# Kernel tuning notes

Measured on AMD Instinct MI355X. Metric: run time of the kernel, lower is better.

Reference implementation:

```python
import jax, jax.numpy as jnp
import numpy as np

B, S, D_MODEL = 2, 2048, 1024
N_HEADS, N_KV_HEADS, D_HEAD = 16, 4, 64
N_GROUPS = N_HEADS // N_KV_HEADS
ATTN_SCALE = 1.0 / np.sqrt(D_HEAD)  # qk_scale_factor=1.0
LOGIT_SOFTCAP = 15.0
WINDOW = 256
N_GLOBAL = 4
EPS = 1e-8


def _l2_normalize(x):
    norm = jnp.linalg.norm(x, axis=-1, keepdims=True)
    return x / (norm + EPS)


def _apply_rope(t, cos, sin):
    # t: (B, H, S, D); cos/sin: (S, D//2)
    half = t.shape[-1] // 2
    x1, x2 = t[..., :half], t[..., half:]
    c = cos[None, None, :, :]
    s = sin[None, None, :, :]
    return jnp.concatenate([x1 * c - x2 * s, x1 * s + x2 * c], axis=-1)


def _sliding_window_mask(seq_len, window, n_global):
    q = jnp.arange(seq_len)[:, None]
    k = jnp.arange(seq_len)[None, :]
    causal = k <= q
    in_window = k > q - window
    is_global = k < n_global
    return (causal & in_window | is_global)[None, None, :, :]


def setup_inputs() -> dict:
    key = jax.random.key(0)
    ks = jax.random.split(key, 7)
    x = jax.random.normal(ks[0], (B, S, D_MODEL), dtype=jnp.float32)
    # RoPE tables from standard inverse-frequency construction
    inv_freq = 1.0 / (10000.0 ** (jnp.arange(0, D_HEAD, 2, dtype=jnp.float32) / D_HEAD))
    angles = jnp.arange(S, dtype=jnp.float32)[:, None] * inv_freq[None, :]  # (S, D_HEAD//2)
    cos = jnp.cos(angles)
    sin = jnp.sin(angles)
    # causal mask supplied by caller (TransformerLM): (1,1,S,S) bool, True = attend
    mask = (jnp.arange(S)[None, :] <= jnp.arange(S)[:, None])[None, None, :, :]
    scale_in = 1.0 / np.sqrt(D_MODEL)
    Wq = jax.random.normal(ks[1], (D_MODEL, N_HEADS * D_HEAD), dtype=jnp.float32) * scale_in
    Wk = jax.random.normal(ks[2], (D_MODEL, N_KV_HEADS * D_HEAD), dtype=jnp.float32) * scale_in
    Wv = jax.random.normal(ks[3], (D_MODEL, N_KV_HEADS * D_HEAD), dtype=jnp.float32) * scale_in
    Wo = jax.random.normal(ks[4], (N_HEADS * D_HEAD, D_MODEL), dtype=jnp.float32) * (1.0 / np.sqrt(N_HEADS * D_HEAD))
    return {"x": x, "cos": cos, "sin": sin, "mask": mask, "Wq": Wq, "Wk": Wk, "Wv": Wv, "Wo": Wo}


def reference(x, cos, sin, mask, Wq, Wk, Wv, Wo):
    Bb, Ss, _ = x.shape
    q = (x @ Wq).reshape(Bb, Ss, N_HEADS, D_HEAD).transpose(0, 2, 1, 3)      # (B,H,S,D)
    k = (x @ Wk).reshape(Bb, Ss, N_KV_HEADS, D_HEAD).transpose(0, 2, 1, 3)   # (B,Hkv,S,D)
    v = (x @ Wv).reshape(Bb, Ss, N_KV_HEADS, D_HEAD).transpose(0, 2, 1, 3)
    # QK L2 normalization (in fp32)
    q = _l2_normalize(q.astype(jnp.float32)).astype(q.dtype)
    k = _l2_normalize(k.astype(jnp.float32)).astype(k.dtype)
    # RoPE
    q = _apply_rope(q, cos, sin)
    k = _apply_rope(k, cos, sin)
    # GQA: expand kv heads
    k_exp = jnp.repeat(k, N_GROUPS, axis=1)
    v_exp = jnp.repeat(v, N_GROUPS, axis=1)
    scores = jnp.einsum('bhqd,bhkd->bhqk', q.astype(jnp.float32), k_exp.astype(jnp.float32)) * ATTN_SCALE
    scores = LOGIT_SOFTCAP * jnp.tanh(scores / LOGIT_SOFTCAP)
    window_mask = _sliding_window_mask(Ss, WINDOW, N_GLOBAL)
    combined = mask & window_mask
    scores = jnp.where(combined, scores, jnp.float32(-1e9))
    weights = jax.nn.softmax(scores, axis=-1)
    context = jnp.einsum('bhqk,bhkd->bhqd', weights, v_exp.astype(jnp.float32))
    context = context.transpose(0, 2, 1, 3).reshape(Bb, Ss, N_HEADS * D_HEAD).astype(x.dtype)
    return context @ Wo
```

## Files before the change

### kernel.cpp

```cpp
#include <hip/hip_runtime.h>
#include <hip/hip_bf16.h>

#define BATCH 2
#define SLEN 2048
#define DMODEL 1024
#define NHEADS 16
#define NKV 4
#define DHEAD 64
#define WINDOW 256
#define NGLOBAL 4

typedef __attribute__((ext_vector_type(8))) short short8;
typedef __attribute__((ext_vector_type(4))) float floatx4;

__device__ __forceinline__ ushort f2bf(float f) {
    __hip_bfloat16 h = __float2bfloat16(f);
    return *reinterpret_cast<ushort*>(&h);
}
__device__ __forceinline__ float bf2f(ushort u) {
    __hip_bfloat16 h = *reinterpret_cast<__hip_bfloat16*>(&u);
    return __bfloat162float(h);
}
__device__ __forceinline__ bool is_bf16_inputs(const uint* cosu) {
    return (cosu[0] & 0xFFFFu) != 0u;
}
__device__ __forceinline__ void gload_lds16(const ushort* g, ushort* l) {
    __builtin_amdgcn_global_load_lds(
        (const __attribute__((address_space(1))) void*)g,
        (__attribute__((address_space(3))) void*)l, 16, 0, 0);
}

__device__ __forceinline__ void stage_row(const ushort* gbase, size_t gstride, int k0,
                                          ushort* lds, int call, int lane) {
    const int c2 = call * 64 + lane;
    const int srow = c2 / 9;
    const int rem = c2 - srow * 9;
    const int colu = (rem == 8) ? 0 : rem * 8;
    gload_lds16(&gbase[(size_t)srow * gstride + k0 + colu], &lds[call * 512]);
}

__global__ __launch_bounds__(256) void prep_all(const void* __restrict__ x,
                                                const void* __restrict__ cosi,
                                                const void* __restrict__ sini,
                                                const void* __restrict__ Wq,
                                                const void* __restrict__ Wk,
                                                const void* __restrict__ Wv,
                                                const void* __restrict__ Wo,
                                                ushort* __restrict__ xb,
                                                float* __restrict__ cosf,
                                                float* __restrict__ sinf,
                                                ushort* __restrict__ Wt,
                                                ushort* __restrict__ Wot,
                                                const uint* __restrict__ cosu)
{
    __shared__ ushort t[32][33];
    const bool isbf = is_bf16_inputs(cosu);
    const int bid = blockIdx.x, tid = threadIdx.x;
    if (bid < 2048) {
        size_t i = (size_t)bid * 256 + tid;
        size_t e = i * 8;
        if (isbf) {
            *reinterpret_cast<uint4*>(xb + e) = reinterpret_cast<const uint4*>(x)[i];
        } else {
            const float* f = reinterpret_cast<const float*>(x) + e;
            ushort o[8];
#pragma unroll
            for (int j = 0; j < 8; ++j) o[j] = f2bf(f[j]);
            *reinterpret_cast<uint4*>(xb + e) = *reinterpret_cast<uint4*>(o);
        }
        return;
    }
    if (bid < 2560) {
        int i = (bid - 2048) * 256 + tid;
        const void* src = (i < SLEN * 32) ? cosi : sini;
        float* dst = (i < SLEN * 32) ? cosf : sinf;
        int e = i & (SLEN * 32 - 1);
        dst[e] = isbf ? bf2f(reinterpret_cast<const ushort*>(src)[e])
                      : reinterpret_cast<const float*>(src)[e];
        return;
    }
    const void* src; ushort* dst; int C, tl;
    if (bid < 3584)      { src = Wq; dst = Wt;                       C = 1024; tl = bid - 2560; }
    else if (bid < 3840) { src = Wk; dst = Wt + (size_t)1024 * 1024; C = 256;  tl = bid - 3584; }
    else if (bid < 4096) { src = Wv; dst = Wt + (size_t)1280 * 1024; C = 256;  tl = bid - 3840; }
    else                 { src = Wo; dst = Wot;                      C = 1024; tl = bid - 4096; }
    const int nbx = C >> 5;
    const int bx = (tl % nbx) * 32, by = (tl / nbx) * 32;
    const int tx = tid & 31, ty = tid >> 5;
#pragma unroll
    for (int j = 0; j < 32; j += 8) {
        size_t idx = (size_t)(by + ty + j) * C + bx + tx;
        t[ty + j][tx] = isbf ? reinterpret_cast<const ushort*>(src)[idx]
                             : f2bf(reinterpret_cast<const float*>(src)[idx]);
    }
    __syncthreads();
#pragma unroll
    for (int j = 0; j < 32; j += 8)
        dst[(size_t)(bx + ty + j) * 1024 + by + tx] = t[tx][ty + j];
}

__global__ __launch_bounds__(256) void gemm_qkv_nr(const ushort* __restrict__ A,
                                                   const ushort* __restrict__ Bt,
                                                   const float* __restrict__ cosf,
                                                   const float* __restrict__ sinf,
                                                   ushort* __restrict__ Qb,
                                                   ushort* __restrict__ Kg,
                                                   ushort* __restrict__ Vtg)
{
    __shared__ __align__(16) ushort sm[13824];
    ushort* lsA = sm;
    ushort* lsB = sm + 9216;
    const int tid = threadIdx.x;
    const int lane = tid & 63, w = tid >> 6;
    const int ln15 = lane & 15, quad = lane >> 4;
    const int z = blockIdx.x;
    const int rm = blockIdx.y * 128;
    const int cn = z * 64;

    floatx4 acc[2][4];
#pragma unroll
    for (int i = 0; i < 2; ++i)
#pragma unroll
        for (int j = 0; j < 4; ++j) acc[i][j] = (floatx4){0.f, 0.f, 0.f, 0.f};

    const ushort* Ab = A + (size_t)rm * 1024;
    const ushort* Bb = Bt + (size_t)cn * 1024;

    for (int k0 = 0; k0 < 1024; k0 += 64) {
        __syncthreads();
#pragma unroll
        for (int i = 0; i < 5; ++i) {
            const int call = i * 4 + w;
            if (call < 18) stage_row(Ab, 1024, k0, lsA, call, lane);
        }
#pragma unroll
        for (int i = 0; i < 3; ++i) {
            const int call = i * 4 + w;
            if (call < 9) stage_row(Bb, 1024, k0, lsB, call, lane);
        }
        __syncthreads();
#pragma unroll
        for (int kk = 0; kk < 64; kk += 32) {
            short8 af[2], bv[4];
#pragma unroll
            for (int i = 0; i < 2; ++i)
                af[i] = *reinterpret_cast<const short8*>(&lsA[(w * 32 + i * 16 + ln15) * 72 + kk + quad * 8]);
#pragma unroll
            for (int j = 0; j < 4; ++j)
                bv[j] = *reinterpret_cast<const short8*>(&lsB[(j * 16 + ln15) * 72 + kk + quad * 8]);
#pragma unroll
            for (int i = 0; i < 2; ++i)
#pragma unroll
                for (int j = 0; j < 4; ++j)
                    acc[i][j] = __builtin_amdgcn_mfma_f32_16x16x32_bf16(af[i], bv[j], acc[i][j], 0, 0, 0);
        }
    }

    __syncthreads();
    const int b = rm >> 11, s0 = rm & (SLEN - 1);
    if (z < 20) {
#pragma unroll
        for (int i = 0; i < 2; ++i) {
#pragma unroll
            for (int r = 0; r < 4; ++r) {
                const int row_l = w * 32 + i * 16 + quad * 4 + r;
                float v0 = acc[i][0][r], v1 = acc[i][1][r], v2 = acc[i][2][r], v3 = acc[i][3][r];
                float ss = v0 * v0 + v1 * v1 + v2 * v2 + v3 * v3;
                ss += __shfl_xor(ss, 1, 64);
                ss += __shfl_xor(ss, 2, 64);
                ss += __shfl_xor(ss, 4, 64);
                ss += __shfl_xor(ss, 8, 64);
                const float inv = 1.f / (sqrtf(ss) + 1e-8f);
                const float n0 = v0 * inv, n1 = v1 * inv, n2 = v2 * inv, n3 = v3 * inv;
                const int spos = s0 + row_l;
                const float c0 = cosf[spos * 32 + ln15],  c1 = cosf[spos * 32 + 16 + ln15];
                const float sn0 = sinf[spos * 32 + ln15], sn1 = sinf[spos * 32 + 16 + ln15];
                sm[row_l * 72 + ln15]      = f2bf(n0 * c0 - n2 * sn0);
                sm[row_l * 72 + 16 + ln15] = f2bf(n1 * c1 - n3 * sn1);
                sm[row_l * 72 + 32 + ln15] = f2bf(n0 * sn0 + n2 * c0);
                sm[row_l * 72 + 48 + ln15] = f2bf(n1 * sn1 + n3 * c1);
            }
        }
        __syncthreads();
        ushort* dst = (z < 16) ? Qb + ((size_t)(b * NHEADS + z) * SLEN + s0) * 64
                               : Kg + ((size_t)(b * NKV + (z - 16)) * SLEN + s0) * 64;
#pragma unroll
        for (int it = 0; it < 4; ++it) {
            const int c = it * 256 + tid;
            const int row = c >> 3, col = (c & 7) * 8;
            *reinterpret_cast<uint4*>(dst + (size_t)row * 64 + col) =
                *reinterpret_cast<const uint4*>(&sm[row * 72 + col]);
        }
    } else {
#pragma unroll
        for (int i = 0; i < 2; ++i)
#pragma unroll
            for (int r = 0; r < 4; ++r) {
                const int row_l = w * 32 + i * 16 + quad * 4 + r;
#pragma unroll
                for (int j = 0; j < 4; ++j)
                    sm[(j * 16 + ln15) * 136 + row_l] = f2bf(acc[i][j][r]);
            }
        __syncthreads();
        ushort* dst = Vtg + ((size_t)(b * NKV + (z - 20)) * 64) * SLEN;
#pragma unroll
        for (int it = 0; it < 4; ++it) {
            const int c = it * 256 + tid;
            const int d = c >> 4, sb = (c & 15) * 8;
            *reinterpret_cast<uint4*>(dst + (size_t)d * SLEN + s0 + sb) =
                *reinterpret_cast<const uint4*>(&sm[d * 136 + sb]);
        }
    }
}

__global__ __launch_bounds__(256) void attn_mfma(const ushort* __restrict__ Qb,
                                                 const ushort* __restrict__ Kg,
                                                 const ushort* __restrict__ Vtg,
                                                 ushort* __restrict__ ctx)
{
    __shared__ ushort Ks[64 * 72];
    __shared__ ushort Vs[64 * 72];
    __shared__ ushort Ps[4][16 * 72];

    const int tid = threadIdx.x;
    const int lane = tid & 63, w = tid >> 6;
    const int ln15 = lane & 15, quad = lane >> 4;
    const int bid = blockIdx.x;
    const int qt = bid & 31, bh = bid >> 5;
    const int h = bh & (NHEADS - 1), b = bh >> 4, hkv = h >> 2;
    const int q0 = qt * 64;
    const int qw = q0 + w * 16;

    const ushort* Qrow = Qb + ((size_t)bh * SLEN + qw) * 64;
    const ushort* Kbase = Kg + (size_t)(b * NKV + hkv) * SLEN * 64;
    const ushort* Vbase = Vtg + (size_t)(b * NKV + hkv) * 64 * SLEN;

    short8 qf0 = *reinterpret_cast<const short8*>(Qrow + (size_t)ln15 * 64 + quad * 8);
    short8 qf1 = *reinterpret_cast<const short8*>(Qrow + (size_t)ln15 * 64 + 32 + quad * 8);

    floatx4 O0 = {0,0,0,0}, O1 = {0,0,0,0}, O2 = {0,0,0,0}, O3 = {0,0,0,0};
    float lp[4] = {0.f, 0.f, 0.f, 0.f};

    int kminA = q0 - (WINDOW - 1); if (kminA < 0) kminA = 0;
    kminA &= ~63;
    const int gmax = kminA < NGLOBAL ? kminA : NGLOBAL;
    const int nc = (q0 + 64 - kminA) >> 6;

    for (int c = (gmax > 0 ? -1 : 0); c < nc; ++c) {
        const int kbase = (c < 0) ? 0 : kminA + c * 64;
        __syncthreads();
#pragma unroll
        for (int j = 0; j < 2; ++j) {
            const int c2 = tid + j * 256;
            const int row = c2 >> 3, col = (c2 & 7) * 8;
            *reinterpret_cast<uint4*>(&Ks[row * 72 + col]) =
                *reinterpret_cast<const uint4*>(&Kbase[(size_t)(kbase + row) * 64 + col]);
            *reinterpret_cast<uint4*>(&Vs[row * 72 + col]) =
                *reinterpret_cast<const uint4*>(&Vbase[(size_t)row * SLEN + kbase + col]);
        }
        __syncthreads();

#pragma unroll
        for (int t = 0; t < 4; ++t) {
            short8 kf0 = *reinterpret_cast<const short8*>(&Ks[(t * 16 + ln15) * 72 + quad * 8]);
            short8 kf1 = *reinterpret_cast<const short8*>(&Ks[(t * 16 + ln15) * 72 + 32 + quad * 8]);
            floatx4 sc = {0,0,0,0};
            sc = __builtin_amdgcn_mfma_f32_16x16x32_bf16(qf0, kf0, sc, 0, 0, 0);
            sc = __builtin_amdgcn_mfma_f32_16x16x32_bf16(qf1, kf1, sc, 0, 0, 0);
            const int k = kbase + t * 16 + ln15;
#pragma unroll
            for (int r = 0; r < 4; ++r) {
                const int q = qw + quad * 4 + r;
                const bool valid = (c < 0) ? (k < gmax)
                                           : (k <= q && (k + WINDOW > q || k < NGLOBAL));
                float sv = sc[r] * 0.125f;
                float st = sv - sv * sv * sv * (1.0f / 675.0f);
                float p = __expf(st);
                Ps[w][(quad * 4 + r) * 72 + t * 16 + ln15] = valid ? f2bf(p) : (ushort)0;
                lp[r] += valid ? p : 0.f;
            }
        }
        short8 af0 = *reinterpret_cast<const short8*>(&Ps[w][ln15 * 72 + quad * 8]);
        short8 af1 = *reinterpret_cast<const short8*>(&Ps[w][ln15 * 72 + 32 + quad * 8]);
#pragma unroll
        for (int n = 0; n < 4; ++n) {
            short8 vf0 = *reinterpret_cast<const short8*>(&Vs[(n * 16 + ln15) * 72 + quad * 8]);
            short8 vf1 = *reinterpret_cast<const short8*>(&Vs[(n * 16 + ln15) * 72 + 32 + quad * 8]);
            floatx4 On = (n == 0) ? O0 : (n == 1) ? O1 : (n == 2) ? O2 : O3;
            On = __builtin_amdgcn_mfma_f32_16x16x32_bf16(af0, vf0, On, 0, 0, 0);
            On = __builtin_amdgcn_mfma_f32_16x16x32_bf16(af1, vf1, On, 0, 0, 0);
            if (n == 0) O0 = On; else if (n == 1) O1 = On; else if (n == 2) O2 = On; else O3 = On;
        }
    }

#pragma unroll
    for (int r = 0; r < 4; ++r) {
#pragma unroll
        for (int off = 1; off < 16; off <<= 1)
            lp[r] += __shfl_xor(lp[r], off, 64);
        const float inv = __builtin_amdgcn_rcpf(lp[r]);
        const int q = qw + quad * 4 + r;
        ushort* crow = ctx + ((size_t)(b * SLEN + q)) * DMODEL + h * 64 + ln15;
        crow[0]  = f2bf(O0[r] * inv);
        crow[16] = f2bf(O1[r] * inv);
        crow[32] = f2bf(O2[r] * inv);
        crow[48] = f2bf(O3[r] * inv);
    }
}

__global__ __launch_bounds__(256) void gemm_out(const ushort* __restrict__ A,
                                                const ushort* __restrict__ Bt,
                                                void* __restrict__ out,
                                                const uint* __restrict__ cosu)
{
    __shared__ __align__(16) ushort sm[13824];
    ushort* lsA = sm;
    ushort* lsB = sm + 9216;
    const int tid = threadIdx.x;
    const int lane = tid & 63, w = tid >> 6;
    const int ln15 = lane & 15, quad = lane >> 4;
    const int rm = blockIdx.y * 128;
    const int cn = blockIdx.x * 64;

    floatx4 acc[2][4];
#pragma unroll
    for (int i = 0; i < 2; ++i)
#pragma unroll
        for (int j = 0; j < 4; ++j) acc[i][j] = (floatx4){0.f, 0.f, 0.f, 0.f};

    const ushort* Ab = A + (size_t)rm * 1024;
    const ushort* Bb = Bt + (size_t)cn * 1024;

    for (int k0 = 0; k0 < 1024; k0 += 64) {
        __syncthreads();
#pragma unroll
        for (int i = 0; i < 5; ++i) {
            const int call = i * 4 + w;
            if (call < 18) stage_row(Ab, 1024, k0, lsA, call, lane);
        }
#pragma unroll
        for (int i = 0; i < 3; ++i) {
            const int call = i * 4 + w;
            if (call < 9) stage_row(Bb, 1024, k0, lsB, call, lane);
        }
        __syncthreads();
#pragma unroll
        for (int kk = 0; kk < 64; kk += 32) {
            short8 af[2], bv[4];
#pragma unroll
            for (int i = 0; i < 2; ++i)
                af[i] = *reinterpret_cast<const short8*>(&lsA[(w * 32 + i * 16 + ln15) * 72 + kk + quad * 8]);
#pragma unroll
            for (int j = 0; j < 4; ++j)
                bv[j] = *reinterpret_cast<const short8*>(&lsB[(j * 16 + ln15) * 72 + kk + quad * 8]);
#pragma unroll
            for (int i = 0; i < 2; ++i)
#pragma unroll
                for (int j = 0; j < 4; ++j)
                    acc[i][j] = __builtin_amdgcn_mfma_f32_16x16x32_bf16(af[i], bv[j], acc[i][j], 0, 0, 0);
        }
    }

    const bool outbf = is_bf16_inputs(cosu);
#pragma unroll
    for (int i = 0; i < 2; ++i) {
#pragma unroll
        for (int r = 0; r < 4; ++r) {
            const int grow = rm + w * 32 + i * 16 + quad * 4 + r;
#pragma unroll
            for (int j = 0; j < 4; ++j) {
                const int gcol = cn + j * 16 + ln15;
                if (outbf) reinterpret_cast<ushort*>(out)[(size_t)grow * DMODEL + gcol] = f2bf(acc[i][j][r]);
                else       reinterpret_cast<float*>(out)[(size_t)grow * DMODEL + gcol] = acc[i][j][r];
            }
        }
    }
}

extern "C" void kernel_launch(void* const* d_in, const int* in_sizes, int n_in,
                              void* d_out, int out_size, void* d_ws, size_t ws_size,
                              hipStream_t stream)
{
    (void)in_sizes; (void)n_in; (void)out_size; (void)ws_size;
    const void* x = d_in[0];
    const void* cosi = d_in[1];
    const void* sini = d_in[2];
    const uint* cosu = (const uint*)d_in[1];
    const void* Wq = d_in[4];
    const void* Wk = d_in[5];
    const void* Wv = d_in[6];
    const void* Wo = d_in[7];

    ushort* xb = (ushort*)d_ws;
    ushort* Wt = xb + (size_t)4096 * 1024;
    ushort* Wot = Wt + (size_t)1536 * 1024;
    float* cosf = (float*)(Wot + (size_t)1024 * 1024);
    float* sinf = cosf + (size_t)SLEN * 32;
    ushort* Qbf = (ushort*)(sinf + (size_t)SLEN * 32);
    ushort* Kgf = Qbf + (size_t)BATCH * NHEADS * SLEN * 64;
    ushort* Vtg = Kgf + (size_t)BATCH * NKV * SLEN * 64;
    ushort* ctx = Vtg + (size_t)BATCH * NKV * 64 * SLEN;

    prep_all<<<dim3(5120), 256, 0, stream>>>(x, cosi, sini, Wq, Wk, Wv, Wo,
                                             xb, cosf, sinf, Wt, Wot, cosu);

    gemm_qkv_nr<<<dim3(24, 32), 256, 0, stream>>>(xb, Wt, cosf, sinf, Qbf, Kgf, Vtg);

    attn_mfma<<<dim3(BATCH * NHEADS * SLEN / 64), 256, 0, stream>>>(Qbf, Kgf, Vtg, ctx);

    gemm_out<<<dim3(16, 32), 256, 0, stream>>>(ctx, Wot, d_out, cosu);
}
```

Measured before the change: 155.1 us.

## Fuse input conversion and weight transpose into GEMMs, add unmasked fast path in attention

Removes the separate prep kernel that converted x, cos/sin and the weights to bf16 and transposed the weights. The QKV and output GEMMs now read the fp32 inputs directly, converting and transposing tiles into LDS as they load them, and the RoPE epilogue reads cos/sin directly. The attention kernel stages K/V with async global-to-LDS loads and takes a mask-free path for fully valid tiles. This saves a kernel launch and a round trip through workspace memory, but the fp32 loads are uncoalesced and scalar. The transposed LDS stores may hit bank conflicts, and every GEMM block now repeats the conversion work.

```diff
diff --git a/kernel.cpp b/kernel.cpp
--- a/kernel.cpp
+++ b/kernel.cpp
@@ -39,73 +39,33 @@
     gload_lds16(&gbase[(size_t)srow * gstride + k0 + colu], &lds[call * 512]);
 }
 
-__global__ __launch_bounds__(256) void prep_all(const void* __restrict__ x,
-                                                const void* __restrict__ cosi,
-                                                const void* __restrict__ sini,
-                                                const void* __restrict__ Wq,
-                                                const void* __restrict__ Wk,
-                                                const void* __restrict__ Wv,
-                                                const void* __restrict__ Wo,
-                                                ushort* __restrict__ xb,
-                                                float* __restrict__ cosf,
-                                                float* __restrict__ sinf,
-                                                ushort* __restrict__ Wt,
-                                                ushort* __restrict__ Wot,
-                                                const uint* __restrict__ cosu)
-{
-    __shared__ ushort t[32][33];
-    const bool isbf = is_bf16_inputs(cosu);
-    const int bid = blockIdx.x, tid = threadIdx.x;
-    if (bid < 2048) {
-        size_t i = (size_t)bid * 256 + tid;
-        size_t e = i * 8;
-        if (isbf) {
-            *reinterpret_cast<uint4*>(xb + e) = reinterpret_cast<const uint4*>(x)[i];
-        } else {
-            const float* f = reinterpret_cast<const float*>(x) + e;
-            ushort o[8];
-#pragma unroll
-            for (int j = 0; j < 8; ++j) o[j] = f2bf(f[j]);
-            *reinterpret_cast<uint4*>(xb + e) = *reinterpret_cast<uint4*>(o);
-        }
-        return;
-    }
-    if (bid < 2560) {
-        int i = (bid - 2048) * 256 + tid;
-        const void* src = (i < SLEN * 32) ? cosi : sini;
-        float* dst = (i < SLEN * 32) ? cosf : sinf;
-        int e = i & (SLEN * 32 - 1);
-        dst[e] = isbf ? bf2f(reinterpret_cast<const ushort*>(src)[e])
-                      : reinterpret_cast<const float*>(src)[e];
-        return;
-    }
-    const void* src; ushort* dst; int C, tl;
-    if (bid < 3584)      { src = Wq; dst = Wt;                       C = 1024; tl = bid - 2560; }
-    else if (bid < 3840) { src = Wk; dst = Wt + (size_t)1024 * 1024; C = 256;  tl = bid - 3584; }
-    else if (bid < 4096) { src = Wv; dst = Wt + (size_t)1280 * 1024; C = 256;  tl = bid - 3840; }
-    else                 { src = Wo; dst = Wot;                      C = 1024; tl = bid - 4096; }
-    const int nbx = C >> 5;
-    const int bx = (tl % nbx) * 32, by = (tl / nbx) * 32;
-    const int tx = tid & 31, ty = tid >> 5;
-#pragma unroll
-    for (int j = 0; j < 32; j += 8) {
-        size_t idx = (size_t)(by + ty + j) * C + bx + tx;
-        t[ty + j][tx] = isbf ? reinterpret_cast<const ushort*>(src)[idx]
-                             : f2bf(reinterpret_cast<const float*>(src)[idx]);
-    }
-    __syncthreads();
-#pragma unroll
-    for (int j = 0; j < 32; j += 8)
-        dst[(size_t)(bx + ty + j) * 1024 + by + tx] = t[tx][ty + j];
-}
-
-__global__ __launch_bounds__(256) void gemm_qkv_nr(const ushort* __restrict__ A,
-                                                   const ushort* __restrict__ Bt,
-                                                   const float* __restrict__ cosf,
-                                                   const float* __restrict__ sinf,
+__device__ __forceinline__ void stage_wT(const void* W, bool isbf, int N, int cn,
+                                         int k0, int ncol, int lane, ushort* lsB) {
+    ushort v[8];
+    if (isbf) {
+        const ushort* Ws = reinterpret_cast<const ushort*>(W);
+        uint4 raw = *reinterpret_cast<const uint4*>(&Ws[(size_t)(k0 + lane) * N + cn + ncol]);
+        *reinterpret_cast<uint4*>(v) = raw;
+    } else {
+        const float* Wf = reinterpret_cast<const float*>(W);
+        const float* p = &Wf[(size_t)(k0 + lane) * N + cn + ncol];
+#pragma unroll
+        for (int i = 0; i < 8; ++i) v[i] = f2bf(p[i]);
+    }
+#pragma unroll
+    for (int i = 0; i < 8; ++i) lsB[(ncol + i) * 72 + lane] = v[i];
+}
+
+__global__ __launch_bounds__(256) void gemm_qkv_nr(const void* __restrict__ x,
+                                                   const void* __restrict__ cosi,
+                                                   const void* __restrict__ sini,
+                                                   const void* __restrict__ Wq,
+                                                   const void* __restrict__ Wk,
+                                                   const void* __restrict__ Wv,
                                                    ushort* __restrict__ Qb,
                                                    ushort* __restrict__ Kg,
-                                                   ushort* __restrict__ Vtg)
+                                                   ushort* __restrict__ Vtg,
+                                                   const uint* __restrict__ cosu)
 {
     __shared__ __align__(16) ushort sm[13824];
     ushort* lsA = sm;
@@ -115,7 +75,12 @@
     const int ln15 = lane & 15, quad = lane >> 4;
     const int z = blockIdx.x;
     const int rm = blockIdx.y * 128;
-    const int cn = z * 64;
+    const bool isbf = is_bf16_inputs(cosu);
+
+    const void* Wsrc; int N, cn;
+    if (z < 16)      { Wsrc = Wq; N = 1024; cn = z * 64; }
+    else if (z < 20) { Wsrc = Wk; N = 256;  cn = (z - 16) * 64; }
+    else             { Wsrc = Wv; N = 256;  cn = (z - 20) * 64; }
 
     floatx4 acc[2][4];
 #pragma unroll
@@ -123,21 +88,31 @@
 #pragma unroll
         for (int j = 0; j < 4; ++j) acc[i][j] = (floatx4){0.f, 0.f, 0.f, 0.f};
 
-    const ushort* Ab = A + (size_t)rm * 1024;
-    const ushort* Bb = Bt + (size_t)cn * 1024;
+    const ushort* xb16 = reinterpret_cast<const ushort*>(x) + (size_t)rm * 1024;
+    const float* xf32 = reinterpret_cast<const float*>(x) + (size_t)rm * 1024;
 
     for (int k0 = 0; k0 < 1024; k0 += 64) {
         __syncthreads();
-#pragma unroll
-        for (int i = 0; i < 5; ++i) {
-            const int call = i * 4 + w;
-            if (call < 18) stage_row(Ab, 1024, k0, lsA, call, lane);
-        }
-#pragma unroll
-        for (int i = 0; i < 3; ++i) {
-            const int call = i * 4 + w;
-            if (call < 9) stage_row(Bb, 1024, k0, lsB, call, lane);
-        }
+        if (isbf) {
+#pragma unroll
+            for (int i = 0; i < 5; ++i) {
+                const int call = i * 4 + w;
+                if (call < 18) stage_row(xb16, 1024, k0, lsA, call, lane);
+            }
+        } else {
+#pragma unroll
+            for (int j = 0; j < 4; ++j) {
+                const int c = tid + j * 256;
+                const int srow = c >> 3, col = (c & 7) * 8;
+                const float* p = &xf32[(size_t)srow * 1024 + k0 + col];
+                ushort o[8];
+#pragma unroll
+                for (int i = 0; i < 8; ++i) o[i] = f2bf(p[i]);
+                *reinterpret_cast<uint4*>(&lsA[srow * 72 + col]) = *reinterpret_cast<uint4*>(o);
+            }
+        }
+        stage_wT(Wsrc, isbf, N, cn, k0, w * 8, lane, lsB);
+        stage_wT(Wsrc, isbf, N, cn, k0, (w + 4) * 8, lane, lsB);
         __syncthreads();
 #pragma unroll
         for (int kk = 0; kk < 64; kk += 32) {
@@ -159,6 +134,10 @@
     __syncthreads();
     const int b = rm >> 11, s0 = rm & (SLEN - 1);
     if (z < 20) {
+        const ushort* cosb = reinterpret_cast<const ushort*>(cosi);
+        const ushort* sinb = reinterpret_cast<const ushort*>(sini);
+        const float* cosF = reinterpret_cast<const float*>(cosi);
+        const float* sinF = reinterpret_cast<const float*>(sini);
 #pragma unroll
         for (int i = 0; i < 2; ++i) {
 #pragma unroll
@@ -173,8 +152,14 @@
                 const float inv = 1.f / (sqrtf(ss) + 1e-8f);
                 const float n0 = v0 * inv, n1 = v1 * inv, n2 = v2 * inv, n3 = v3 * inv;
                 const int spos = s0 + row_l;
-                const float c0 = cosf[spos * 32 + ln15],  c1 = cosf[spos * 32 + 16 + ln15];
-                const float sn0 = sinf[spos * 32 + ln15], sn1 = sinf[spos * 32 + 16 + ln15];
+                float c0, c1, sn0, sn1;
+                if (isbf) {
+                    c0 = bf2f(cosb[spos * 32 + ln15]);  c1 = bf2f(cosb[spos * 32 + 16 + ln15]);
+                    sn0 = bf2f(sinb[spos * 32 + ln15]); sn1 = bf2f(sinb[spos * 32 + 16 + ln15]);
+                } else {
+                    c0 = cosF[spos * 32 + ln15];  c1 = cosF[spos * 32 + 16 + ln15];
+                    sn0 = sinF[spos * 32 + ln15]; sn1 = sinF[spos * 32 + 16 + ln15];
+                }
                 sm[row_l * 72 + ln15]      = f2bf(n0 * c0 - n2 * sn0);
                 sm[row_l * 72 + 16 + ln15] = f2bf(n1 * c1 - n3 * sn1);
                 sm[row_l * 72 + 32 + ln15] = f2bf(n0 * sn0 + n2 * c0);
@@ -218,13 +203,13 @@
                                                  const ushort* __restrict__ Vtg,
                                                  ushort* __restrict__ ctx)
 {
-    __shared__ ushort Ks[64 * 72];
-    __shared__ ushort Vs[64 * 72];
-    __shared__ ushort Ps[4][16 * 72];
-
+    __shared__ __align__(16) ushort sm[13824];
+    ushort* Ks = sm;
+    ushort* Vs = sm + 4608;
     const int tid = threadIdx.x;
     const int lane = tid & 63, w = tid >> 6;
     const int ln15 = lane & 15, quad = lane >> 4;
+    ushort* Ps = sm + 9216 + w * 1152;
     const int bid = blockIdx.x;
     const int qt = bid & 31, bh = bid >> 5;
     const int h = bh & (NHEADS - 1), b = bh >> 4, hkv = h >> 2;
@@ -250,38 +235,59 @@
         const int kbase = (c < 0) ? 0 : kminA + c * 64;
         __syncthreads();
 #pragma unroll
-        for (int j = 0; j < 2; ++j) {
-            const int c2 = tid + j * 256;
-            const int row = c2 >> 3, col = (c2 & 7) * 8;
-            *reinterpret_cast<uint4*>(&Ks[row * 72 + col]) =
-                *reinterpret_cast<const uint4*>(&Kbase[(size_t)(kbase + row) * 64 + col]);
-            *reinterpret_cast<uint4*>(&Vs[row * 72 + col]) =
-                *reinterpret_cast<const uint4*>(&Vbase[(size_t)row * SLEN + kbase + col]);
-        }
-        __syncthreads();
-
-#pragma unroll
-        for (int t = 0; t < 4; ++t) {
-            short8 kf0 = *reinterpret_cast<const short8*>(&Ks[(t * 16 + ln15) * 72 + quad * 8]);
-            short8 kf1 = *reinterpret_cast<const short8*>(&Ks[(t * 16 + ln15) * 72 + 32 + quad * 8]);
-            floatx4 sc = {0,0,0,0};
-            sc = __builtin_amdgcn_mfma_f32_16x16x32_bf16(qf0, kf0, sc, 0, 0, 0);
-            sc = __builtin_amdgcn_mfma_f32_16x16x32_bf16(qf1, kf1, sc, 0, 0, 0);
-            const int k = kbase + t * 16 + ln15;
-#pragma unroll
-            for (int r = 0; r < 4; ++r) {
-                const int q = qw + quad * 4 + r;
-                const bool valid = (c < 0) ? (k < gmax)
-                                           : (k <= q && (k + WINDOW > q || k < NGLOBAL));
-                float sv = sc[r] * 0.125f;
-                float st = sv - sv * sv * sv * (1.0f / 675.0f);
-                float p = __expf(st);
-                Ps[w][(quad * 4 + r) * 72 + t * 16 + ln15] = valid ? f2bf(p) : (ushort)0;
-                lp[r] += valid ? p : 0.f;
-            }
-        }
-        short8 af0 = *reinterpret_cast<const short8*>(&Ps[w][ln15 * 72 + quad * 8]);
-        short8 af1 = *reinterpret_cast<const short8*>(&Ps[w][ln15 * 72 + 32 + quad * 8]);
+        for (int i = 0; i < 3; ++i) {
+            const int call = i * 4 + w;
+            if (call < 9) stage_row(Kbase + (size_t)kbase * 64, 64, 0, Ks, call, lane);
+        }
+#pragma unroll
+        for (int i = 0; i < 3; ++i) {
+            const int call = i * 4 + w;
+            if (call < 9) stage_row(Vbase + kbase, SLEN, 0, Vs, call, lane);
+        }
+        __syncthreads();
+
+        const bool allvalid = (c >= 0) && (kbase + 63 <= qw) && (kbase + WINDOW >= qw + 16);
+        if (allvalid) {
+#pragma unroll
+            for (int t = 0; t < 4; ++t) {
+                short8 kf0 = *reinterpret_cast<const short8*>(&Ks[(t * 16 + ln15) * 72 + quad * 8]);
+                short8 kf1 = *reinterpret_cast<const short8*>(&Ks[(t * 16 + ln15) * 72 + 32 + quad * 8]);
+                floatx4 sc = {0,0,0,0};
+                sc = __builtin_amdgcn_mfma_f32_16x16x32_bf16(qf0, kf0, sc, 0, 0, 0);
+                sc = __builtin_amdgcn_mfma_f32_16x16x32_bf16(qf1, kf1, sc, 0, 0, 0);
+#pragma unroll
+                for (int r = 0; r < 4; ++r) {
+                    float sv = sc[r] * 0.125f;
+                    float st = sv - sv * sv * sv * (1.0f / 675.0f);
+                    float p = __expf(st);
+                    Ps[(quad * 4 + r) * 72 + t * 16 + ln15] = f2bf(p);
+                    lp[r] += p;
+                }
+            }
+        } else {
+#pragma unroll
+            for (int t = 0; t < 4; ++t) {
+                short8 kf0 = *reinterpret_cast<const short8*>(&Ks[(t * 16 + ln15) * 72 + quad * 8]);
+                short8 kf1 = *reinterpret_cast<const short8*>(&Ks[(t * 16 + ln15) * 72 + 32 + quad * 8]);
+                floatx4 sc = {0,0,0,0};
+                sc = __builtin_amdgcn_mfma_f32_16x16x32_bf16(qf0, kf0, sc, 0, 0, 0);
+                sc = __builtin_amdgcn_mfma_f32_16x16x32_bf16(qf1, kf1, sc, 0, 0, 0);
+                const int k = kbase + t * 16 + ln15;
+#pragma unroll
+                for (int r = 0; r < 4; ++r) {
+                    const int q = qw + quad * 4 + r;
+                    const bool valid = (c < 0) ? (k < gmax)
+                                               : (k <= q && (k + WINDOW > q || k < NGLOBAL));
+                    float sv = sc[r] * 0.125f;
+                    float st = sv - sv * sv * sv * (1.0f / 675.0f);
+                    float p = __expf(st);
+                    Ps[(quad * 4 + r) * 72 + t * 16 + ln15] = valid ? f2bf(p) : (ushort)0;
+                    lp[r] += valid ? p : 0.f;
+                }
+            }
+        }
+        short8 af0 = *reinterpret_cast<const short8*>(&Ps[ln15 * 72 + quad * 8]);
+        short8 af1 = *reinterpret_cast<const short8*>(&Ps[ln15 * 72 + 32 + quad * 8]);
 #pragma unroll
         for (int n = 0; n < 4; ++n) {
             short8 vf0 = *reinterpret_cast<const short8*>(&Vs[(n * 16 + ln15) * 72 + quad * 8]);
@@ -309,7 +315,7 @@
 }
 
 __global__ __launch_bounds__(256) void gemm_out(const ushort* __restrict__ A,
-                                                const ushort* __restrict__ Bt,
+                                                const void* __restrict__ Wo,
                                                 void* __restrict__ out,
                                                 const uint* __restrict__ cosu)
 {
@@ -321,6 +327,7 @@
     const int ln15 = lane & 15, quad = lane >> 4;
     const int rm = blockIdx.y * 128;
     const int cn = blockIdx.x * 64;
+    const bool isbf = is_bf16_inputs(cosu);
 
     floatx4 acc[2][4];
 #pragma unroll
@@ -329,7 +336,6 @@
         for (int j = 0; j < 4; ++j) acc[i][j] = (floatx4){0.f, 0.f, 0.f, 0.f};
 
     const ushort* Ab = A + (size_t)rm * 1024;
-    const ushort* Bb = Bt + (size_t)cn * 1024;
 
     for (int k0 = 0; k0 < 1024; k0 += 64) {
         __syncthreads();
@@ -338,11 +344,8 @@
             const int call = i * 4 + w;
             if (call < 18) stage_row(Ab, 1024, k0, lsA, call, lane);
         }
-#pragma unroll
-        for (int i = 0; i < 3; ++i) {
-            const int call = i * 4 + w;
-            if (call < 9) stage_row(Bb, 1024, k0, lsB, call, lane);
-        }
+        stage_wT(Wo, isbf, 1024, cn, k0, w * 8, lane, lsB);
+        stage_wT(Wo, isbf, 1024, cn, k0, (w + 4) * 8, lane, lsB);
         __syncthreads();
 #pragma unroll
         for (int kk = 0; kk < 64; kk += 32) {
@@ -361,7 +364,6 @@
         }
     }
 
-    const bool outbf = is_bf16_inputs(cosu);
 #pragma unroll
     for (int i = 0; i < 2; ++i) {
 #pragma unroll
@@ -370,8 +372,8 @@
 #pragma unroll
             for (int j = 0; j < 4; ++j) {
                 const int gcol = cn + j * 16 + ln15;
-                if (outbf) reinterpret_cast<ushort*>(out)[(size_t)grow * DMODEL + gcol] = f2bf(acc[i][j][r]);
-                else       reinterpret_cast<float*>(out)[(size_t)grow * DMODEL + gcol] = acc[i][j][r];
+                if (isbf) reinterpret_cast<ushort*>(out)[(size_t)grow * DMODEL + gcol] = f2bf(acc[i][j][r]);
+                else      reinterpret_cast<float*>(out)[(size_t)grow * DMODEL + gcol] = acc[i][j][r];
             }
         }
     }
@@ -391,22 +393,15 @@
     const void* Wv = d_in[6];
     const void* Wo = d_in[7];
 
-    ushort* xb = (ushort*)d_ws;
-    ushort* Wt = xb + (size_t)4096 * 1024;
-    ushort* Wot = Wt + (size_t)1536 * 1024;
-    float* cosf = (float*)(Wot + (size_t)1024 * 1024);
-    float* sinf = cosf + (size_t)SLEN * 32;
-    ushort* Qbf = (ushort*)(sinf + (size_t)SLEN * 32);
+    ushort* Qbf = (ushort*)d_ws;
     ushort* Kgf = Qbf + (size_t)BATCH * NHEADS * SLEN * 64;
     ushort* Vtg = Kgf + (size_t)BATCH * NKV * SLEN * 64;
     ushort* ctx = Vtg + (size_t)BATCH * NKV * 64 * SLEN;
 
-    prep_all<<<dim3(5120), 256, 0, stream>>>(x, cosi, sini, Wq, Wk, Wv, Wo,
-                                             xb, cosf, sinf, Wt, Wot, cosu);
-
-    gemm_qkv_nr<<<dim3(24, 32), 256, 0, stream>>>(xb, Wt, cosf, sinf, Qbf, Kgf, Vtg);
+    gemm_qkv_nr<<<dim3(24, 32), 256, 0, stream>>>(x, cosi, sini, Wq, Wk, Wv,
+                                                  Qbf, Kgf, Vtg, cosu);
 
     attn_mfma<<<dim3(BATCH * NHEADS * SLEN / 64), 256, 0, stream>>>(Qbf, Kgf, Vtg, ctx);
 
-    gemm_out<<<dim3(16, 32), 256, 0, stream>>>(ctx, Wot, d_out, cosu);
-}
+    gemm_out<<<dim3(16, 32), 256, 0, stream>>>(ctx, Wo, d_out, cosu);
+}
```

Measured after the change: 186.8 us. 1.2x slower.

## Skip x copy for bf16 inputs, use stage_row in attention, fast path unmasked tiles

Applied to the files above, without the earlier changes.

When the inputs are bf16, the prep kernel no longer copies x into a workspace buffer, and the QKV GEMM reads x directly. The attention kernel now stages K and V tiles with the shared stage_row helper and a unified shared-memory buffer. It also adds a branch that skips per-element mask evaluation for tiles that are entirely inside the causal window. The inputs are fp32 by default, so the x-copy skip likely does not run. The mask fast path adds code size and divergence risk.

```diff
diff --git a/kernel.cpp b/kernel.cpp
--- a/kernel.cpp
+++ b/kernel.cpp
@@ -57,17 +57,14 @@
     const bool isbf = is_bf16_inputs(cosu);
     const int bid = blockIdx.x, tid = threadIdx.x;
     if (bid < 2048) {
+        if (isbf) return;
         size_t i = (size_t)bid * 256 + tid;
         size_t e = i * 8;
-        if (isbf) {
-            *reinterpret_cast<uint4*>(xb + e) = reinterpret_cast<const uint4*>(x)[i];
-        } else {
-            const float* f = reinterpret_cast<const float*>(x) + e;
-            ushort o[8];
-#pragma unroll
-            for (int j = 0; j < 8; ++j) o[j] = f2bf(f[j]);
-            *reinterpret_cast<uint4*>(xb + e) = *reinterpret_cast<uint4*>(o);
-        }
+        const float* f = reinterpret_cast<const float*>(x) + e;
+        ushort o[8];
+#pragma unroll
+        for (int j = 0; j < 8; ++j) o[j] = f2bf(f[j]);
+        *reinterpret_cast<uint4*>(xb + e) = *reinterpret_cast<uint4*>(o);
         return;
     }
     if (bid < 2560) {
@@ -99,13 +96,15 @@
         dst[(size_t)(bx + ty + j) * 1024 + by + tx] = t[tx][ty + j];
 }
 
-__global__ __launch_bounds__(256) void gemm_qkv_nr(const ushort* __restrict__ A,
+__global__ __launch_bounds__(256) void gemm_qkv_nr(const void* __restrict__ x,
+                                                   const ushort* __restrict__ xb,
                                                    const ushort* __restrict__ Bt,
                                                    const float* __restrict__ cosf,
                                                    const float* __restrict__ sinf,
                                                    ushort* __restrict__ Qb,
                                                    ushort* __restrict__ Kg,
-                                                   ushort* __restrict__ Vtg)
+                                                   ushort* __restrict__ Vtg,
+                                                   const uint* __restrict__ cosu)
 {
     __shared__ __align__(16) ushort sm[13824];
     ushort* lsA = sm;
@@ -116,6 +115,7 @@
     const int z = blockIdx.x;
     const int rm = blockIdx.y * 128;
     const int cn = z * 64;
+    const bool isbf = is_bf16_inputs(cosu);
 
     floatx4 acc[2][4];
 #pragma unroll
@@ -123,7 +123,7 @@
 #pragma unroll
         for (int j = 0; j < 4; ++j) acc[i][j] = (floatx4){0.f, 0.f, 0.f, 0.f};
 
-    const ushort* Ab = A + (size_t)rm * 1024;
+    const ushort* Ab = (isbf ? reinterpret_cast<const ushort*>(x) : xb) + (size_t)rm * 1024;
     const ushort* Bb = Bt + (size_t)cn * 1024;
 
     for (int k0 = 0; k0 < 1024; k0 += 64) {
@@ -218,13 +218,13 @@
                                                  const ushort* __restrict__ Vtg,
                                                  ushort* __restrict__ ctx)
 {
-    __shared__ ushort Ks[64 * 72];
-    __shared__ ushort Vs[64 * 72];
-    __shared__ ushort Ps[4][16 * 72];
-
+    __shared__ __align__(16) ushort sm[13824];
+    ushort* Ks = sm;
+    ushort* Vs = sm + 4608;
     const int tid = threadIdx.x;
     const int lane = tid & 63, w = tid >> 6;
     const int ln15 = lane & 15, quad = lane >> 4;
+    ushort* Ps = sm + 9216 + w * 1152;
     const int bid = blockIdx.x;
     const int qt = bid & 31, bh = bid >> 5;
     const int h = bh & (NHEADS - 1), b = bh >> 4, hkv = h >> 2;
@@ -250,38 +250,59 @@
         const int kbase = (c < 0) ? 0 : kminA + c * 64;
         __syncthreads();
 #pragma unroll
-        for (int j = 0; j < 2; ++j) {
-            const int c2 = tid + j * 256;
-            const int row = c2 >> 3, col = (c2 & 7) * 8;
-            *reinterpret_cast<uint4*>(&Ks[row * 72 + col]) =
-                *reinterpret_cast<const uint4*>(&Kbase[(size_t)(kbase + row) * 64 + col]);
-            *reinterpret_cast<uint4*>(&Vs[row * 72 + col]) =
-                *reinterpret_cast<const uint4*>(&Vbase[(size_t)row * SLEN + kbase + col]);
-        }
-        __syncthreads();
-
-#pragma unroll
-        for (int t = 0; t < 4; ++t) {
-            short8 kf0 = *reinterpret_cast<const short8*>(&Ks[(t * 16 + ln15) * 72 + quad * 8]);
-            short8 kf1 = *reinterpret_cast<const short8*>(&Ks[(t * 16 + ln15) * 72 + 32 + quad * 8]);
-            floatx4 sc = {0,0,0,0};
-            sc = __builtin_amdgcn_mfma_f32_16x16x32_bf16(qf0, kf0, sc, 0, 0, 0);
-            sc = __builtin_amdgcn_mfma_f32_16x16x32_bf16(qf1, kf1, sc, 0, 0, 0);
-            const int k = kbase + t * 16 + ln15;
-#pragma unroll
-            for (int r = 0; r < 4; ++r) {
-                const int q = qw + quad * 4 + r;
-                const bool valid = (c < 0) ? (k < gmax)
-                                           : (k <= q && (k + WINDOW > q || k < NGLOBAL));
-                float sv = sc[r] * 0.125f;
-                float st = sv - sv * sv * sv * (1.0f / 675.0f);
-                float p = __expf(st);
-                Ps[w][(quad * 4 + r) * 72 + t * 16 + ln15] = valid ? f2bf(p) : (ushort)0;
-                lp[r] += valid ? p : 0.f;
+        for (int i = 0; i < 3; ++i) {
+            const int call = i * 4 + w;
+            if (call < 9) stage_row(Kbase + (size_t)kbase * 64, 64, 0, Ks, call, lane);
+        }
+#pragma unroll
+        for (int i = 0; i < 3; ++i) {
+            const int call = i * 4 + w;
+            if (call < 9) stage_row(Vbase + kbase, SLEN, 0, Vs, call, lane);
+        }
+        __syncthreads();
+
+        const bool allvalid = (c >= 0) && (kbase + 63 <= qw) && (kbase + WINDOW >= qw + 16);
+        if (allvalid) {
+#pragma unroll
+            for (int t = 0; t < 4; ++t) {
+                short8 kf0 = *reinterpret_cast<const short8*>(&Ks[(t * 16 + ln15) * 72 + quad * 8]);
+                short8 kf1 = *reinterpret_cast<const short8*>(&Ks[(t * 16 + ln15) * 72 + 32 + quad * 8]);
+                floatx4 sc = {0,0,0,0};
+                sc = __builtin_amdgcn_mfma_f32_16x16x32_bf16(qf0, kf0, sc, 0, 0, 0);
+                sc = __builtin_amdgcn_mfma_f32_16x16x32_bf16(qf1, kf1, sc, 0, 0, 0);
+#pragma unroll
+                for (int r = 0; r < 4; ++r) {
+                    float sv = sc[r] * 0.125f;
+                    float st = sv - sv * sv * sv * (1.0f / 675.0f);
+                    float p = __expf(st);
+                    Ps[(quad * 4 + r) * 72 + t * 16 + ln15] = f2bf(p);
+                    lp[r] += p;
+                }
             }
-        }
-        short8 af0 = *reinterpret_cast<const short8*>(&Ps[w][ln15 * 72 + quad * 8]);
-        short8 af1 = *reinterpret_cast<const short8*>(&Ps[w][ln15 * 72 + 32 + quad * 8]);
+        } else {
+#pragma unroll
+            for (int t = 0; t < 4; ++t) {
+                short8 kf0 = *reinterpret_cast<const short8*>(&Ks[(t * 16 + ln15) * 72 + quad * 8]);
+                short8 kf1 = *reinterpret_cast<const short8*>(&Ks[(t * 16 + ln15) * 72 + 32 + quad * 8]);
+                floatx4 sc = {0,0,0,0};
+                sc = __builtin_amdgcn_mfma_f32_16x16x32_bf16(qf0, kf0, sc, 0, 0, 0);
+                sc = __builtin_amdgcn_mfma_f32_16x16x32_bf16(qf1, kf1, sc, 0, 0, 0);
+                const int k = kbase + t * 16 + ln15;
+#pragma unroll
+                for (int r = 0; r < 4; ++r) {
+                    const int q = qw + quad * 4 + r;
+                    const bool valid = (c < 0) ? (k < gmax)
+                                               : (k <= q && (k + WINDOW > q || k < NGLOBAL));
+                    float sv = sc[r] * 0.125f;
+                    float st = sv - sv * sv * sv * (1.0f / 675.0f);
+                    float p = __expf(st);
+                    Ps[(quad * 4 + r) * 72 + t * 16 + ln15] = valid ? f2bf(p) : (ushort)0;
+                    lp[r] += valid ? p : 0.f;
+                }
+            }
+        }
+        short8 af0 = *reinterpret_cast<const short8*>(&Ps[ln15 * 72 + quad * 8]);
+        short8 af1 = *reinterpret_cast<const short8*>(&Ps[ln15 * 72 + 32 + quad * 8]);
 #pragma unroll
         for (int n = 0; n < 4; ++n) {
             short8 vf0 = *reinterpret_cast<const short8*>(&Vs[(n * 16 + ln15) * 72 + quad * 8]);
@@ -404,7 +425,8 @@
     prep_all<<<dim3(5120), 256, 0, stream>>>(x, cosi, sini, Wq, Wk, Wv, Wo,
                                              xb, cosf, sinf, Wt, Wot, cosu);
 
-    gemm_qkv_nr<<<dim3(24, 32), 256, 0, stream>>>(xb, Wt, cosf, sinf, Qbf, Kgf, Vtg);
+    gemm_qkv_nr<<<dim3(24, 32), 256, 0, stream>>>(x, xb, Wt, cosf, sinf,
+                                                  Qbf, Kgf, Vtg, cosu);
 
     attn_mfma<<<dim3(BATCH * NHEADS * SLEN / 64), 256, 0, stream>>>(Qbf, Kgf, Vtg, ctx);
 
```

New measurement: 154.1 us. About the same (-0.6%).
